# Kernel optimization log

Hardware: AMD Instinct MI355X
Metric: run time of the kernel (lower is better)

The kernel has to match this reference:

```python
import jax, jax.numpy as jnp
import numpy as np

S = 8192  # sequence length
D = 256   # feature dim


def setup_inputs() -> dict:
    key = jax.random.key(0)
    kq, kk, kv = jax.random.split(key, 3)
    Q = jax.random.normal(kq, (S, D), dtype=jnp.float32)
    K = jax.random.normal(kk, (S, D), dtype=jnp.float32)
    V = jax.random.normal(kv, (S, D), dtype=jnp.float32)
    return {"Q": Q, "K": K, "V": V}


def reference(Q, K, V):
    # Faithful to the torch module: dk = K.size(-2) (the SEQUENCE length, not head dim)
    dk = K.shape[-2]
    scores = (Q @ K.T) / jnp.sqrt(jnp.float32(dk))  # [S, S]
    # F.softmax with implicit dim on a 2D tensor -> softmax over last dim (keys)
    attn = jax.nn.softmax(scores, axis=-1)
    return attn @ V  # [S, D]
```

## Files before the change

### kernel.cpp

```cpp
#include <hip/hip_runtime.h>


typedef __attribute__((ext_vector_type(4))) float    f32x4;
typedef __attribute__((ext_vector_type(4))) int      i32x4;
typedef __attribute__((ext_vector_type(2))) long     lx2;
typedef __attribute__((ext_vector_type(2))) _Float16 h2;
typedef __attribute__((ext_vector_type(2))) __fp16   h2raw;
typedef __attribute__((ext_vector_type(8))) _Float16 h8;
typedef long  __attribute__((may_alias)) long_a;
typedef lx2   __attribute__((may_alias)) lx2_a;
typedef h8    __attribute__((may_alias)) h8_a;

#define SEQ 8192
#define DIM 256
#define NSPLIT 8
#define KPS (SEQ / NSPLIT)
#define BN 32
#define ITERS (KPS / BN)
#define BM 128

#define KSC (1.4426950408889634f / 90.50966799187808f)

#define KTILE 8192
#define VTILE 16384
#define BUFSZ (KTILE + VTILE)

__global__ void __launch_bounds__(256)
prep(const float* __restrict__ Q, const float* __restrict__ K,
     const float* __restrict__ V, unsigned char* __restrict__ Q8,
     unsigned char* __restrict__ K8, _Float16* __restrict__ Vt) {
    __shared__ _Float16 tile[32][264];
    int b = blockIdx.x, t = threadIdx.x;

    {
        int row = b * 32 + (t >> 3);
        int c0 = (t & 7) * 8;
        const f32x4* q4 = (const f32x4*)Q + (size_t)row * 64 + c0;
        const f32x4* k4 = (const f32x4*)K + (size_t)row * 64 + c0;
        int qo[8], ko[8];
        #pragma unroll
        for (int i = 0; i < 8; ++i) {
            f32x4 q = q4[i], k = k4[i];
            int dq = 0, dk = 0;
            dq = __builtin_amdgcn_cvt_pk_fp8_f32(q.x, q.y, dq, false);
            dq = __builtin_amdgcn_cvt_pk_fp8_f32(q.z, q.w, dq, true);
            dk = __builtin_amdgcn_cvt_pk_fp8_f32(k.x, k.y, dk, false);
            dk = __builtin_amdgcn_cvt_pk_fp8_f32(k.z, k.w, dk, true);
            qo[i] = dq; ko[i] = dk;
        }
        i32x4* qd = (i32x4*)(Q8 + (size_t)row * 256 + (t & 7) * 32);
        qd[0] = *(i32x4*)&qo[0]; qd[1] = *(i32x4*)&qo[4];

        int s16h = (((t & 7) >> 1) << 1) + (t >> 7);
        long* kdst = (long*)(K8 + (size_t)b * KTILE + (size_t)s16h * 1024
                             + (size_t)((t >> 3) & 15) * 16 + (size_t)(t & 1) * 8);
        #pragma unroll
        for (int q = 0; q < 4; ++q) kdst[q * 32] = *(const long*)&ko[2 * q];
    }

    #pragma unroll
    for (int i = 0; i < 8; ++i) {
        int c = t + i * 256;
        int row = c >> 6, col = c & 63;
        f32x4 v = ((const f32x4*)V)[(size_t)(b * 32 + row) * 64 + col];
        tile[row][col * 4 + 0] = (_Float16)v.x;
        tile[row][col * 4 + 1] = (_Float16)v.y;
        tile[row][col * 4 + 2] = (_Float16)v.z;
        tile[row][col * 4 + 3] = (_Float16)v.w;
    }
    __syncthreads();
    _Float16* dst = Vt + (size_t)b * 8192 + (size_t)t * 8;
    #pragma unroll
    for (int a = 0; a < 4; ++a) {
        h8 w;
        #pragma unroll
        for (int j = 0; j < 4; ++j) {
            w[j]     = tile[4 * a + j][t];
            w[4 + j] = tile[16 + 4 * a + j][t];
        }
        *(h8_a*)(dst + (size_t)a * 2048) = w;
    }
}

__device__ __forceinline__ void gl16(const void* g, void* l) {
    __builtin_amdgcn_global_load_lds(
        (const __attribute__((address_space(1))) void*)g,
        (__attribute__((address_space(3))) void*)l, 16, 0, 0);
}

__device__ __forceinline__ h2 pkrtz(float a, float b) {
    h2raw r = __builtin_amdgcn_cvt_pkrtz(a, b);
    return __builtin_bit_cast(h2, r);
}

__device__ __forceinline__ void qk32(const unsigned char* kb, int koff,
                                     const long (&qf)[2][8], f32x4 (&sc)[2][2]) {
    #pragma unroll
    for (int h = 0; h < 2; ++h)
        #pragma unroll
        for (int t = 0; t < 2; ++t) sc[h][t] = (f32x4){0.f, 0.f, 0.f, 0.f};
    #pragma unroll
    for (int s16 = 0; s16 < 4; ++s16) {
        #pragma unroll
        for (int h = 0; h < 2; ++h) {
            lx2 kp = *(const lx2_a*)(kb + (s16 * 2 + h) * 1024 + koff);
            #pragma unroll
            for (int t = 0; t < 2; ++t) {
                sc[h][t] = __builtin_amdgcn_mfma_f32_16x16x32_fp8_fp8(kp[0], qf[t][2 * s16],     sc[h][t], 0, 0, 0);
                sc[h][t] = __builtin_amdgcn_mfma_f32_16x16x32_fp8_fp8(kp[1], qf[t][2 * s16 + 1], sc[h][t], 0, 0, 0);
            }
        }
    }
}

#define STAGE(KG, VG, BUF)                                                   \
    do {                                                                     \
        gl16((KG) + tid * 16,           (BUF) + wb);                         \
        gl16((KG) + 4096 + tid * 16,    (BUF) + 4096 + wb);                  \
        gl16((VG) + tid * 16,           (BUF) + KTILE + wb);                 \
        gl16((VG) + 4096 + tid * 16,    (BUF) + KTILE + 4096 + wb);         \
        gl16((VG) + 8192 + tid * 16,    (BUF) + KTILE + 8192 + wb);         \
        gl16((VG) + 12288 + tid * 16,   (BUF) + KTILE + 12288 + wb);        \
    } while (0)

__global__ void __launch_bounds__(256, 2)
attn(const unsigned char* __restrict__ Q8, const unsigned char* __restrict__ K8,
     const _Float16* __restrict__ Vt, _Float16* __restrict__ Op,
     float* __restrict__ lp) {
    __shared__ __align__(16) unsigned char lds[3 * BUFSZ];

    int tid = threadIdx.x;
    int wid = tid >> 6, lane = tid & 63;
    int l15 = lane & 15, qq = lane >> 4;
    int wb = wid << 10;
    int qt_blk = blockIdx.x >> 3, sp = blockIdx.x & 7;
    int qrow0 = qt_blk * BM + wid * 32;

    long qf[2][8];
    #pragma unroll
    for (int t = 0; t < 2; ++t) {
        const unsigned char* p = Q8 + (size_t)(qrow0 + t * 16 + l15) * DIM + qq * 8;
        #pragma unroll
        for (int s = 0; s < 8; ++s) qf[t][s] = *(const long_a*)(p + s * 32);
    }

    _Float16 one = (l15 == 0) ? (_Float16)1.0f : (_Float16)0.0f;
    h8 of = {one, one, one, one, one, one, one, one};

    unsigned char* bufA = lds;
    unsigned char* bufB = lds + BUFSZ;
    unsigned char* bufC = lds + 2 * BUFSZ;

    const unsigned char* kg = K8 + (size_t)sp * ITERS * KTILE;
    const unsigned char* vg = (const unsigned char*)Vt + (size_t)sp * ITERS * VTILE;

    f32x4 acc[2][16] = {};
    f32x4 accl[2] = {};

    int koff = qq * 256 + l15 * 16;
    int voff = qq * 4096 + l15 * 16;

    STAGE(kg, vg, bufA); kg += KTILE; vg += VTILE;
    STAGE(kg, vg, bufB); kg += KTILE; vg += VTILE;
    __syncthreads();
    f32x4 sc_p[2][2];
    qk32(bufA, koff, qf, sc_p);

    for (int it = 0; it < ITERS; ++it) {
        if (it + 2 < ITERS) { STAGE(kg, vg, bufC); kg += KTILE; vg += VTILE; }

        __builtin_amdgcn_s_setprio(1);

        f32x4 sc_n[2][2] = {};
        if (it + 1 < ITERS) qk32(bufB, koff, qf, sc_n);

        h8 pfrag[2];
        #pragma unroll
        for (int t = 0; t < 2; ++t) {
            float e0 = __builtin_amdgcn_exp2f(fminf(sc_p[0][t][0] * KSC, 16.0f));
            float e1 = __builtin_amdgcn_exp2f(fminf(sc_p[0][t][1] * KSC, 16.0f));
            float e2 = __builtin_amdgcn_exp2f(fminf(sc_p[0][t][2] * KSC, 16.0f));
            float e3 = __builtin_amdgcn_exp2f(fminf(sc_p[0][t][3] * KSC, 16.0f));
            float e4 = __builtin_amdgcn_exp2f(fminf(sc_p[1][t][0] * KSC, 16.0f));
            float e5 = __builtin_amdgcn_exp2f(fminf(sc_p[1][t][1] * KSC, 16.0f));
            float e6 = __builtin_amdgcn_exp2f(fminf(sc_p[1][t][2] * KSC, 16.0f));
            float e7 = __builtin_amdgcn_exp2f(fminf(sc_p[1][t][3] * KSC, 16.0f));
            h2 p01 = pkrtz(e0, e1);
            h2 p23 = pkrtz(e2, e3);
            h2 p45 = pkrtz(e4, e5);
            h2 p67 = pkrtz(e6, e7);
            h8 pf;
            pf[0] = p01[0]; pf[1] = p01[1]; pf[2] = p23[0]; pf[3] = p23[1];
            pf[4] = p45[0]; pf[5] = p45[1]; pf[6] = p67[0]; pf[7] = p67[1];
            pfrag[t] = pf;
        }

        const unsigned char* vb = bufA + KTILE + voff;
        #pragma unroll
        for (int n = 0; n < 16; ++n) {
            h8 vf = *(const h8_a*)(vb + n * 256);
            acc[0][n] = __builtin_amdgcn_mfma_f32_16x16x32_f16(pfrag[0], vf, acc[0][n], 0, 0, 0);
            acc[1][n] = __builtin_amdgcn_mfma_f32_16x16x32_f16(pfrag[1], vf, acc[1][n], 0, 0, 0);
        }
        accl[0] = __builtin_amdgcn_mfma_f32_16x16x32_f16(pfrag[0], of, accl[0], 0, 0, 0);
        accl[1] = __builtin_amdgcn_mfma_f32_16x16x32_f16(pfrag[1], of, accl[1], 0, 0, 0);

        __builtin_amdgcn_s_setprio(0);
        __syncthreads();

        unsigned char* tb = bufA; bufA = bufB; bufB = bufC; bufC = tb;
        #pragma unroll
        for (int h = 0; h < 2; ++h)
            #pragma unroll
            for (int t = 0; t < 2; ++t) sc_p[h][t] = sc_n[h][t];
    }

    #pragma unroll
    for (int t = 0; t < 2; ++t) {
        #pragma unroll
        for (int n = 0; n < 16; ++n)
            #pragma unroll
            for (int r = 0; r < 4; ++r) {
                int row = qrow0 + t * 16 + qq * 4 + r;
                Op[((size_t)sp * SEQ + row) * DIM + n * 16 + l15] = (_Float16)acc[t][n][r];
            }
        if (l15 == 0) {
            #pragma unroll
            for (int r = 0; r < 4; ++r)
                lp[(size_t)sp * SEQ + qrow0 + t * 16 + qq * 4 + r] = accl[t][r];
        }
    }
}

__global__ void __launch_bounds__(256)
combine(const _Float16* __restrict__ Op, const float* __restrict__ lp,
        float* __restrict__ out) {
    int idx = blockIdx.x * 256 + threadIdx.x;
    int row = idx >> 5;
    f32x4 a0 = {}, a1 = {};
    float l = 0.0f;
    #pragma unroll
    for (int s = 0; s < NSPLIT; ++s) {
        h8 h = *(const h8_a*)(Op + (size_t)s * SEQ * DIM + (size_t)idx * 8);
        a0.x += (float)h[0]; a0.y += (float)h[1];
        a0.z += (float)h[2]; a0.w += (float)h[3];
        a1.x += (float)h[4]; a1.y += (float)h[5];
        a1.z += (float)h[6]; a1.w += (float)h[7];
        l += lp[s * SEQ + row];
    }
    float linv = 1.0f / (l + 1e-20f);
    ((f32x4*)out)[idx * 2]     = a0 * linv;
    ((f32x4*)out)[idx * 2 + 1] = a1 * linv;
}

extern "C" void kernel_launch(void* const* d_in, const int* in_sizes, int n_in,
                              void* d_out, int out_size, void* d_ws, size_t ws_size,
                              hipStream_t stream) {
    const float* Q = (const float*)d_in[0];
    const float* K = (const float*)d_in[1];
    const float* V = (const float*)d_in[2];
    float* out = (float*)d_out;

    char* ws = (char*)d_ws;
    unsigned char* Q8 = (unsigned char*)ws;
    unsigned char* K8 = (unsigned char*)(ws + (2u << 20));
    _Float16* Vt = (_Float16*)(ws + (4u << 20));
    _Float16* Op = (_Float16*)(ws + (8u << 20));
    float*    lp = (float*)(ws + (40u << 20));

    prep   <<<256, 256, 0, stream>>>(Q, K, V, Q8, K8, Vt);
    attn   <<<NSPLIT * (SEQ / BM), 256, 0, stream>>>(Q8, K8, Vt, Op, lp);
    combine<<<1024, 256, 0, stream>>>(Op, lp, out);
}
```

Measured before the change: 140.0 us.

## Fuse split-K combine into attention via atomic last-block reduction, use 8 waves

Removes the separate combine kernel. The last split block for each query tile, detected with an atomic counter that prep zeroes, performs the reduction and writes the output. The attention block goes from 4 to 8 waves with 16 query rows per wave, uses double buffering instead of triple, and drops the software-pipelined QK score prefetch. This saves a kernel launch and raises occupancy, at the cost of less overlap between QK and PV inside each wave and a serialized reduction tail in the last block.

```diff
diff --git a/kernel.cpp b/kernel.cpp
--- a/kernel.cpp
+++ b/kernel.cpp
@@ -28,9 +28,12 @@
 __global__ void __launch_bounds__(256)
 prep(const float* __restrict__ Q, const float* __restrict__ K,
      const float* __restrict__ V, unsigned char* __restrict__ Q8,
-     unsigned char* __restrict__ K8, _Float16* __restrict__ Vt) {
+     unsigned char* __restrict__ K8, _Float16* __restrict__ Vt,
+     int* __restrict__ cnt) {
     __shared__ _Float16 tile[32][264];
     int b = blockIdx.x, t = threadIdx.x;
+
+    if (b == 0 && t < 64) cnt[t] = 0;
 
     {
         int row = b * 32 + (t >> 3);
@@ -93,164 +96,136 @@
     return __builtin_bit_cast(h2, r);
 }
 
-__device__ __forceinline__ void qk32(const unsigned char* kb, int koff,
-                                     const long (&qf)[2][8], f32x4 (&sc)[2][2]) {
-    #pragma unroll
-    for (int h = 0; h < 2; ++h)
-        #pragma unroll
-        for (int t = 0; t < 2; ++t) sc[h][t] = (f32x4){0.f, 0.f, 0.f, 0.f};
-    #pragma unroll
-    for (int s16 = 0; s16 < 4; ++s16) {
-        #pragma unroll
-        for (int h = 0; h < 2; ++h) {
-            lx2 kp = *(const lx2_a*)(kb + (s16 * 2 + h) * 1024 + koff);
-            #pragma unroll
-            for (int t = 0; t < 2; ++t) {
-                sc[h][t] = __builtin_amdgcn_mfma_f32_16x16x32_fp8_fp8(kp[0], qf[t][2 * s16],     sc[h][t], 0, 0, 0);
-                sc[h][t] = __builtin_amdgcn_mfma_f32_16x16x32_fp8_fp8(kp[1], qf[t][2 * s16 + 1], sc[h][t], 0, 0, 0);
-            }
-        }
-    }
-}
-
 #define STAGE(KG, VG, BUF)                                                   \
     do {                                                                     \
-        gl16((KG) + tid * 16,           (BUF) + wb);                         \
-        gl16((KG) + 4096 + tid * 16,    (BUF) + 4096 + wb);                  \
-        gl16((VG) + tid * 16,           (BUF) + KTILE + wb);                 \
-        gl16((VG) + 4096 + tid * 16,    (BUF) + KTILE + 4096 + wb);         \
-        gl16((VG) + 8192 + tid * 16,    (BUF) + KTILE + 8192 + wb);         \
-        gl16((VG) + 12288 + tid * 16,   (BUF) + KTILE + 12288 + wb);        \
+        gl16((KG) + tid * 16,          (BUF) + wb);                          \
+        gl16((VG) + tid * 16,          (BUF) + KTILE + wb);                  \
+        gl16((VG) + 8192 + tid * 16,   (BUF) + KTILE + 8192 + wb);          \
     } while (0)
 
-__global__ void __launch_bounds__(256, 2)
+__global__ void __launch_bounds__(512, 4)
 attn(const unsigned char* __restrict__ Q8, const unsigned char* __restrict__ K8,
      const _Float16* __restrict__ Vt, _Float16* __restrict__ Op,
-     float* __restrict__ lp) {
-    __shared__ __align__(16) unsigned char lds[3 * BUFSZ];
+     float* __restrict__ lp, float* __restrict__ out, int* __restrict__ cnt) {
+    __shared__ __align__(16) unsigned char lds[2 * BUFSZ];
+    __shared__ int lastv;
 
     int tid = threadIdx.x;
     int wid = tid >> 6, lane = tid & 63;
     int l15 = lane & 15, qq = lane >> 4;
     int wb = wid << 10;
     int qt_blk = blockIdx.x >> 3, sp = blockIdx.x & 7;
-    int qrow0 = qt_blk * BM + wid * 32;
-
-    long qf[2][8];
-    #pragma unroll
-    for (int t = 0; t < 2; ++t) {
-        const unsigned char* p = Q8 + (size_t)(qrow0 + t * 16 + l15) * DIM + qq * 8;
-        #pragma unroll
-        for (int s = 0; s < 8; ++s) qf[t][s] = *(const long_a*)(p + s * 32);
+    int qrow0 = qt_blk * BM + wid * 16;
+
+    long qf[8];
+    {
+        const unsigned char* p = Q8 + (size_t)(qrow0 + l15) * DIM + qq * 8;
+        #pragma unroll
+        for (int s = 0; s < 8; ++s) qf[s] = *(const long_a*)(p + s * 32);
     }
 
     _Float16 one = (l15 == 0) ? (_Float16)1.0f : (_Float16)0.0f;
     h8 of = {one, one, one, one, one, one, one, one};
 
-    unsigned char* bufA = lds;
-    unsigned char* bufB = lds + BUFSZ;
-    unsigned char* bufC = lds + 2 * BUFSZ;
-
     const unsigned char* kg = K8 + (size_t)sp * ITERS * KTILE;
     const unsigned char* vg = (const unsigned char*)Vt + (size_t)sp * ITERS * VTILE;
 
-    f32x4 acc[2][16] = {};
-    f32x4 accl[2] = {};
+    f32x4 acc[16] = {};
+    f32x4 accl = {};
 
     int koff = qq * 256 + l15 * 16;
     int voff = qq * 4096 + l15 * 16;
 
-    STAGE(kg, vg, bufA); kg += KTILE; vg += VTILE;
-    STAGE(kg, vg, bufB); kg += KTILE; vg += VTILE;
-    __syncthreads();
-    f32x4 sc_p[2][2];
-    qk32(bufA, koff, qf, sc_p);
+    STAGE(kg, vg, lds); kg += KTILE; vg += VTILE;
+    __syncthreads();
 
     for (int it = 0; it < ITERS; ++it) {
-        if (it + 2 < ITERS) { STAGE(kg, vg, bufC); kg += KTILE; vg += VTILE; }
+        unsigned char* buf = lds + (it & 1) * BUFSZ;
+        if (it + 1 < ITERS) {
+            STAGE(kg, vg, lds + ((it + 1) & 1) * BUFSZ);
+            kg += KTILE; vg += VTILE;
+        }
 
         __builtin_amdgcn_s_setprio(1);
 
-        f32x4 sc_n[2][2] = {};
-        if (it + 1 < ITERS) qk32(bufB, koff, qf, sc_n);
-
-        h8 pfrag[2];
-        #pragma unroll
-        for (int t = 0; t < 2; ++t) {
-            float e0 = __builtin_amdgcn_exp2f(fminf(sc_p[0][t][0] * KSC, 16.0f));
-            float e1 = __builtin_amdgcn_exp2f(fminf(sc_p[0][t][1] * KSC, 16.0f));
-            float e2 = __builtin_amdgcn_exp2f(fminf(sc_p[0][t][2] * KSC, 16.0f));
-            float e3 = __builtin_amdgcn_exp2f(fminf(sc_p[0][t][3] * KSC, 16.0f));
-            float e4 = __builtin_amdgcn_exp2f(fminf(sc_p[1][t][0] * KSC, 16.0f));
-            float e5 = __builtin_amdgcn_exp2f(fminf(sc_p[1][t][1] * KSC, 16.0f));
-            float e6 = __builtin_amdgcn_exp2f(fminf(sc_p[1][t][2] * KSC, 16.0f));
-            float e7 = __builtin_amdgcn_exp2f(fminf(sc_p[1][t][3] * KSC, 16.0f));
-            h2 p01 = pkrtz(e0, e1);
-            h2 p23 = pkrtz(e2, e3);
-            h2 p45 = pkrtz(e4, e5);
-            h2 p67 = pkrtz(e6, e7);
-            h8 pf;
-            pf[0] = p01[0]; pf[1] = p01[1]; pf[2] = p23[0]; pf[3] = p23[1];
-            pf[4] = p45[0]; pf[5] = p45[1]; pf[6] = p67[0]; pf[7] = p67[1];
-            pfrag[t] = pf;
-        }
-
-        const unsigned char* vb = bufA + KTILE + voff;
+        f32x4 sc[2] = {};
+        #pragma unroll
+        for (int s16 = 0; s16 < 4; ++s16) {
+            #pragma unroll
+            for (int h = 0; h < 2; ++h) {
+                lx2 kp = *(const lx2_a*)(buf + (s16 * 2 + h) * 1024 + koff);
+                sc[h] = __builtin_amdgcn_mfma_f32_16x16x32_fp8_fp8(kp[0], qf[2 * s16],     sc[h], 0, 0, 0);
+                sc[h] = __builtin_amdgcn_mfma_f32_16x16x32_fp8_fp8(kp[1], qf[2 * s16 + 1], sc[h], 0, 0, 0);
+            }
+        }
+
+        float e0 = __builtin_amdgcn_exp2f(fminf(sc[0][0] * KSC, 16.0f));
+        float e1 = __builtin_amdgcn_exp2f(fminf(sc[0][1] * KSC, 16.0f));
+        float e2 = __builtin_amdgcn_exp2f(fminf(sc[0][2] * KSC, 16.0f));
+        float e3 = __builtin_amdgcn_exp2f(fminf(sc[0][3] * KSC, 16.0f));
+        float e4 = __builtin_amdgcn_exp2f(fminf(sc[1][0] * KSC, 16.0f));
+        float e5 = __builtin_amdgcn_exp2f(fminf(sc[1][1] * KSC, 16.0f));
+        float e6 = __builtin_amdgcn_exp2f(fminf(sc[1][2] * KSC, 16.0f));
+        float e7 = __builtin_amdgcn_exp2f(fminf(sc[1][3] * KSC, 16.0f));
+        h2 p01 = pkrtz(e0, e1);
+        h2 p23 = pkrtz(e2, e3);
+        h2 p45 = pkrtz(e4, e5);
+        h2 p67 = pkrtz(e6, e7);
+        h8 pfrag;
+        pfrag[0] = p01[0]; pfrag[1] = p01[1]; pfrag[2] = p23[0]; pfrag[3] = p23[1];
+        pfrag[4] = p45[0]; pfrag[5] = p45[1]; pfrag[6] = p67[0]; pfrag[7] = p67[1];
+
+        const unsigned char* vb = buf + KTILE + voff;
         #pragma unroll
         for (int n = 0; n < 16; ++n) {
             h8 vf = *(const h8_a*)(vb + n * 256);
-            acc[0][n] = __builtin_amdgcn_mfma_f32_16x16x32_f16(pfrag[0], vf, acc[0][n], 0, 0, 0);
-            acc[1][n] = __builtin_amdgcn_mfma_f32_16x16x32_f16(pfrag[1], vf, acc[1][n], 0, 0, 0);
-        }
-        accl[0] = __builtin_amdgcn_mfma_f32_16x16x32_f16(pfrag[0], of, accl[0], 0, 0, 0);
-        accl[1] = __builtin_amdgcn_mfma_f32_16x16x32_f16(pfrag[1], of, accl[1], 0, 0, 0);
+            acc[n] = __builtin_amdgcn_mfma_f32_16x16x32_f16(pfrag, vf, acc[n], 0, 0, 0);
+        }
+        accl = __builtin_amdgcn_mfma_f32_16x16x32_f16(pfrag, of, accl, 0, 0, 0);
 
         __builtin_amdgcn_s_setprio(0);
         __syncthreads();
-
-        unsigned char* tb = bufA; bufA = bufB; bufB = bufC; bufC = tb;
-        #pragma unroll
-        for (int h = 0; h < 2; ++h)
+    }
+
+    #pragma unroll
+    for (int n = 0; n < 16; ++n)
+        #pragma unroll
+        for (int r = 0; r < 4; ++r) {
+            int row = qrow0 + qq * 4 + r;
+            Op[((size_t)sp * SEQ + row) * DIM + n * 16 + l15] = (_Float16)acc[n][r];
+        }
+    if (l15 == 0) {
+        #pragma unroll
+        for (int r = 0; r < 4; ++r)
+            lp[(size_t)sp * SEQ + qrow0 + qq * 4 + r] = accl[r];
+    }
+
+    __threadfence();
+    __syncthreads();
+    if (tid == 0) lastv = atomicAdd(cnt + qt_blk, 1);
+    __syncthreads();
+    if (lastv == NSPLIT - 1) {
+        __threadfence();
+        #pragma unroll 1
+        for (int c = 0; c < 8; ++c) {
+            int idx = (qt_blk << 12) + (c << 9) + tid;
+            int row = idx >> 5;
+            f32x4 a0 = {}, a1 = {};
+            float l = 0.0f;
             #pragma unroll
-            for (int t = 0; t < 2; ++t) sc_p[h][t] = sc_n[h][t];
-    }
-
-    #pragma unroll
-    for (int t = 0; t < 2; ++t) {
-        #pragma unroll
-        for (int n = 0; n < 16; ++n)
-            #pragma unroll
-            for (int r = 0; r < 4; ++r) {
-                int row = qrow0 + t * 16 + qq * 4 + r;
-                Op[((size_t)sp * SEQ + row) * DIM + n * 16 + l15] = (_Float16)acc[t][n][r];
+            for (int s = 0; s < NSPLIT; ++s) {
+                h8 h = *(const h8_a*)(Op + (size_t)s * SEQ * DIM + (size_t)idx * 8);
+                a0.x += (float)h[0]; a0.y += (float)h[1];
+                a0.z += (float)h[2]; a0.w += (float)h[3];
+                a1.x += (float)h[4]; a1.y += (float)h[5];
+                a1.z += (float)h[6]; a1.w += (float)h[7];
+                l += lp[s * SEQ + row];
             }
-        if (l15 == 0) {
-            #pragma unroll
-            for (int r = 0; r < 4; ++r)
-                lp[(size_t)sp * SEQ + qrow0 + t * 16 + qq * 4 + r] = accl[t][r];
-        }
-    }
-}
-
-__global__ void __launch_bounds__(256)
-combine(const _Float16* __restrict__ Op, const float* __restrict__ lp,
-        float* __restrict__ out) {
-    int idx = blockIdx.x * 256 + threadIdx.x;
-    int row = idx >> 5;
-    f32x4 a0 = {}, a1 = {};
-    float l = 0.0f;
-    #pragma unroll
-    for (int s = 0; s < NSPLIT; ++s) {
-        h8 h = *(const h8_a*)(Op + (size_t)s * SEQ * DIM + (size_t)idx * 8);
-        a0.x += (float)h[0]; a0.y += (float)h[1];
-        a0.z += (float)h[2]; a0.w += (float)h[3];
-        a1.x += (float)h[4]; a1.y += (float)h[5];
-        a1.z += (float)h[6]; a1.w += (float)h[7];
-        l += lp[s * SEQ + row];
-    }
-    float linv = 1.0f / (l + 1e-20f);
-    ((f32x4*)out)[idx * 2]     = a0 * linv;
-    ((f32x4*)out)[idx * 2 + 1] = a1 * linv;
+            float linv = 1.0f / (l + 1e-20f);
+            ((f32x4*)out)[(size_t)idx * 2]     = a0 * linv;
+            ((f32x4*)out)[(size_t)idx * 2 + 1] = a1 * linv;
+        }
+    }
 }
 
 extern "C" void kernel_launch(void* const* d_in, const int* in_sizes, int n_in,
@@ -267,8 +242,8 @@
     _Float16* Vt = (_Float16*)(ws + (4u << 20));
     _Float16* Op = (_Float16*)(ws + (8u << 20));
     float*    lp = (float*)(ws + (40u << 20));
-
-    prep   <<<256, 256, 0, stream>>>(Q, K, V, Q8, K8, Vt);
-    attn   <<<NSPLIT * (SEQ / BM), 256, 0, stream>>>(Q8, K8, Vt, Op, lp);
-    combine<<<1024, 256, 0, stream>>>(Op, lp, out);
-}
+    int*     cnt = (int*)(ws + (40u << 20) + (256u << 10));
+
+    prep<<<256, 256, 0, stream>>>(Q, K, V, Q8, K8, Vt, cnt);
+    attn<<<NSPLIT * (SEQ / BM), 512, 0, stream>>>(Q8, K8, Vt, Op, lp, out, cnt);
+}
```

Measured after the change: 340.2 us. +142.9%, slower.

## Fuse split-K combine into attention kernel via last-block atomic counter

Applied to the files above, without the earlier changes.

Removes the separate combine launch. Each attention block increments a per-query-tile atomic counter after writing its partial output, and the last of the NSPLIT blocks reduces all partials for that tile and writes the final normalized output. Counters are zeroed in the prep kernel. This saves a kernel launch and lets combine work overlap with other tiles' attention, but the last block per tile now does serial reduction work with only 256 threads, which could create a tail.

```diff
diff --git a/kernel.cpp b/kernel.cpp
--- a/kernel.cpp
+++ b/kernel.cpp
@@ -28,9 +28,12 @@
 __global__ void __launch_bounds__(256)
 prep(const float* __restrict__ Q, const float* __restrict__ K,
      const float* __restrict__ V, unsigned char* __restrict__ Q8,
-     unsigned char* __restrict__ K8, _Float16* __restrict__ Vt) {
+     unsigned char* __restrict__ K8, _Float16* __restrict__ Vt,
+     int* __restrict__ cnt) {
     __shared__ _Float16 tile[32][264];
     int b = blockIdx.x, t = threadIdx.x;
+
+    if (b == 0 && t < 64) cnt[t] = 0;
 
     {
         int row = b * 32 + (t >> 3);
@@ -126,8 +129,9 @@
 __global__ void __launch_bounds__(256, 2)
 attn(const unsigned char* __restrict__ Q8, const unsigned char* __restrict__ K8,
      const _Float16* __restrict__ Vt, _Float16* __restrict__ Op,
-     float* __restrict__ lp) {
+     float* __restrict__ lp, float* __restrict__ out, int* __restrict__ cnt) {
     __shared__ __align__(16) unsigned char lds[3 * BUFSZ];
+    __shared__ int lastv;
 
     int tid = threadIdx.x;
     int wid = tid >> 6, lane = tid & 63;
@@ -230,27 +234,33 @@
                 lp[(size_t)sp * SEQ + qrow0 + t * 16 + qq * 4 + r] = accl[t][r];
         }
     }
-}
-
-__global__ void __launch_bounds__(256)
-combine(const _Float16* __restrict__ Op, const float* __restrict__ lp,
-        float* __restrict__ out) {
-    int idx = blockIdx.x * 256 + threadIdx.x;
-    int row = idx >> 5;
-    f32x4 a0 = {}, a1 = {};
-    float l = 0.0f;
-    #pragma unroll
-    for (int s = 0; s < NSPLIT; ++s) {
-        h8 h = *(const h8_a*)(Op + (size_t)s * SEQ * DIM + (size_t)idx * 8);
-        a0.x += (float)h[0]; a0.y += (float)h[1];
-        a0.z += (float)h[2]; a0.w += (float)h[3];
-        a1.x += (float)h[4]; a1.y += (float)h[5];
-        a1.z += (float)h[6]; a1.w += (float)h[7];
-        l += lp[s * SEQ + row];
-    }
-    float linv = 1.0f / (l + 1e-20f);
-    ((f32x4*)out)[idx * 2]     = a0 * linv;
-    ((f32x4*)out)[idx * 2 + 1] = a1 * linv;
+
+    __threadfence();
+    __syncthreads();
+    if (tid == 0) lastv = atomicAdd(cnt + qt_blk, 1);
+    __syncthreads();
+    if (lastv == NSPLIT - 1) {
+        __threadfence();
+        #pragma unroll 1
+        for (int c = 0; c < 16; ++c) {
+            int idx = (qt_blk << 12) + (c << 8) + tid;
+            int row = idx >> 5;
+            f32x4 a0 = {}, a1 = {};
+            float l = 0.0f;
+            #pragma unroll
+            for (int s = 0; s < NSPLIT; ++s) {
+                h8 h = *(const h8_a*)(Op + (size_t)s * SEQ * DIM + (size_t)idx * 8);
+                a0.x += (float)h[0]; a0.y += (float)h[1];
+                a0.z += (float)h[2]; a0.w += (float)h[3];
+                a1.x += (float)h[4]; a1.y += (float)h[5];
+                a1.z += (float)h[6]; a1.w += (float)h[7];
+                l += lp[s * SEQ + row];
+            }
+            float linv = 1.0f / (l + 1e-20f);
+            ((f32x4*)out)[(size_t)idx * 2]     = a0 * linv;
+            ((f32x4*)out)[(size_t)idx * 2 + 1] = a1 * linv;
+        }
+    }
 }
 
 extern "C" void kernel_launch(void* const* d_in, const int* in_sizes, int n_in,
@@ -267,8 +277,8 @@
     _Float16* Vt = (_Float16*)(ws + (4u << 20));
     _Float16* Op = (_Float16*)(ws + (8u << 20));
     float*    lp = (float*)(ws + (40u << 20));
-
-    prep   <<<256, 256, 0, stream>>>(Q, K, V, Q8, K8, Vt);
-    attn   <<<NSPLIT * (SEQ / BM), 256, 0, stream>>>(Q8, K8, Vt, Op, lp);
-    combine<<<1024, 256, 0, stream>>>(Op, lp, out);
-}
+    int*     cnt = (int*)(ws + (40u << 20) + (256u << 10));
+
+    prep<<<256, 256, 0, stream>>>(Q, K, V, Q8, K8, Vt, cnt);
+    attn<<<NSPLIT * (SEQ / BM), 256, 0, stream>>>(Q8, K8, Vt, Op, lp, out, cnt);
+}
```

Result: slower. 246.2 us (+75.9%).

## Load K tiles directly into registers instead of staging through LDS

Applied to the files above, without the earlier changes.

K fragments are now read from global memory straight into registers (prefetched one iteration ahead), and only V tiles are staged into LDS through the triple buffer. This cuts the LDS footprint and the LDS read traffic for the QK MFMAs, and drops the sc_p/sc_n copy by reordering softmax before the next QK. In exchange it adds register pressure from the K prefetch registers and exposes global load latency directly to the waves.

```diff
diff --git a/kernel.cpp b/kernel.cpp
--- a/kernel.cpp
+++ b/kernel.cpp
@@ -23,7 +23,6 @@
 
 #define KTILE 8192
 #define VTILE 16384
-#define BUFSZ (KTILE + VTILE)
 
 __global__ void __launch_bounds__(256)
 prep(const float* __restrict__ Q, const float* __restrict__ K,
@@ -93,8 +92,15 @@
     return __builtin_bit_cast(h2, r);
 }
 
-__device__ __forceinline__ void qk32(const unsigned char* kb, int koff,
-                                     const long (&qf)[2][8], f32x4 (&sc)[2][2]) {
+__device__ __forceinline__ void loadk(const unsigned char* kg, int koff,
+                                      lx2 (&kreg)[8]) {
+    #pragma unroll
+    for (int c = 0; c < 8; ++c)
+        kreg[c] = *(const lx2_a*)(kg + c * 1024 + koff);
+}
+
+__device__ __forceinline__ void qk32r(const lx2 (&kreg)[8], const long (&qf)[2][8],
+                                      f32x4 (&sc)[2][2]) {
     #pragma unroll
     for (int h = 0; h < 2; ++h)
         #pragma unroll
@@ -103,7 +109,7 @@
     for (int s16 = 0; s16 < 4; ++s16) {
         #pragma unroll
         for (int h = 0; h < 2; ++h) {
-            lx2 kp = *(const lx2_a*)(kb + (s16 * 2 + h) * 1024 + koff);
+            lx2 kp = kreg[s16 * 2 + h];
             #pragma unroll
             for (int t = 0; t < 2; ++t) {
                 sc[h][t] = __builtin_amdgcn_mfma_f32_16x16x32_fp8_fp8(kp[0], qf[t][2 * s16],     sc[h][t], 0, 0, 0);
@@ -113,21 +119,53 @@
     }
 }
 
-#define STAGE(KG, VG, BUF)                                                   \
+__device__ __forceinline__ void sm32(const f32x4 (&sc)[2][2], h8 (&pfrag)[2]) {
+    #pragma unroll
+    for (int t = 0; t < 2; ++t) {
+        float e0 = __builtin_amdgcn_exp2f(fminf(sc[0][t][0] * KSC, 16.0f));
+        float e1 = __builtin_amdgcn_exp2f(fminf(sc[0][t][1] * KSC, 16.0f));
+        float e2 = __builtin_amdgcn_exp2f(fminf(sc[0][t][2] * KSC, 16.0f));
+        float e3 = __builtin_amdgcn_exp2f(fminf(sc[0][t][3] * KSC, 16.0f));
+        float e4 = __builtin_amdgcn_exp2f(fminf(sc[1][t][0] * KSC, 16.0f));
+        float e5 = __builtin_amdgcn_exp2f(fminf(sc[1][t][1] * KSC, 16.0f));
+        float e6 = __builtin_amdgcn_exp2f(fminf(sc[1][t][2] * KSC, 16.0f));
+        float e7 = __builtin_amdgcn_exp2f(fminf(sc[1][t][3] * KSC, 16.0f));
+        h2 p01 = pkrtz(e0, e1);
+        h2 p23 = pkrtz(e2, e3);
+        h2 p45 = pkrtz(e4, e5);
+        h2 p67 = pkrtz(e6, e7);
+        h8 pf;
+        pf[0] = p01[0]; pf[1] = p01[1]; pf[2] = p23[0]; pf[3] = p23[1];
+        pf[4] = p45[0]; pf[5] = p45[1]; pf[6] = p67[0]; pf[7] = p67[1];
+        pfrag[t] = pf;
+    }
+}
+
+__device__ __forceinline__ void pv32(const unsigned char* vb, const h8 (&pfrag)[2],
+                                     const h8& of, f32x4 (&acc)[2][16], f32x4 (&accl)[2]) {
+    #pragma unroll
+    for (int n = 0; n < 16; ++n) {
+        h8 vf = *(const h8_a*)(vb + n * 256);
+        acc[0][n] = __builtin_amdgcn_mfma_f32_16x16x32_f16(pfrag[0], vf, acc[0][n], 0, 0, 0);
+        acc[1][n] = __builtin_amdgcn_mfma_f32_16x16x32_f16(pfrag[1], vf, acc[1][n], 0, 0, 0);
+    }
+    accl[0] = __builtin_amdgcn_mfma_f32_16x16x32_f16(pfrag[0], of, accl[0], 0, 0, 0);
+    accl[1] = __builtin_amdgcn_mfma_f32_16x16x32_f16(pfrag[1], of, accl[1], 0, 0, 0);
+}
+
+#define STAGEV(VG, BUF)                                                      \
     do {                                                                     \
-        gl16((KG) + tid * 16,           (BUF) + wb);                         \
-        gl16((KG) + 4096 + tid * 16,    (BUF) + 4096 + wb);                  \
-        gl16((VG) + tid * 16,           (BUF) + KTILE + wb);                 \
-        gl16((VG) + 4096 + tid * 16,    (BUF) + KTILE + 4096 + wb);         \
-        gl16((VG) + 8192 + tid * 16,    (BUF) + KTILE + 8192 + wb);         \
-        gl16((VG) + 12288 + tid * 16,   (BUF) + KTILE + 12288 + wb);        \
+        gl16((VG) + tid * 16,          (BUF) + wb);                          \
+        gl16((VG) + 4096 + tid * 16,   (BUF) + 4096 + wb);                   \
+        gl16((VG) + 8192 + tid * 16,   (BUF) + 8192 + wb);                   \
+        gl16((VG) + 12288 + tid * 16,  (BUF) + 12288 + wb);                  \
     } while (0)
 
 __global__ void __launch_bounds__(256, 2)
 attn(const unsigned char* __restrict__ Q8, const unsigned char* __restrict__ K8,
      const _Float16* __restrict__ Vt, _Float16* __restrict__ Op,
      float* __restrict__ lp) {
-    __shared__ __align__(16) unsigned char lds[3 * BUFSZ];
+    __shared__ __align__(16) unsigned char lds[3 * VTILE];
 
     int tid = threadIdx.x;
     int wid = tid >> 6, lane = tid & 63;
@@ -148,8 +186,8 @@
     h8 of = {one, one, one, one, one, one, one, one};
 
     unsigned char* bufA = lds;
-    unsigned char* bufB = lds + BUFSZ;
-    unsigned char* bufC = lds + 2 * BUFSZ;
+    unsigned char* bufB = lds + VTILE;
+    unsigned char* bufC = lds + 2 * VTILE;
 
     const unsigned char* kg = K8 + (size_t)sp * ITERS * KTILE;
     const unsigned char* vg = (const unsigned char*)Vt + (size_t)sp * ITERS * VTILE;
@@ -160,59 +198,34 @@
     int koff = qq * 256 + l15 * 16;
     int voff = qq * 4096 + l15 * 16;
 
-    STAGE(kg, vg, bufA); kg += KTILE; vg += VTILE;
-    STAGE(kg, vg, bufB); kg += KTILE; vg += VTILE;
+    lx2 kreg[8];
+
+    STAGEV(vg, bufA); vg += VTILE;
+    STAGEV(vg, bufB); vg += VTILE;
+    loadk(kg, koff, kreg); kg += KTILE;
     __syncthreads();
-    f32x4 sc_p[2][2];
-    qk32(bufA, koff, qf, sc_p);
+    f32x4 sc[2][2];
+    qk32r(kreg, qf, sc);
+    loadk(kg, koff, kreg); kg += KTILE;
 
     for (int it = 0; it < ITERS; ++it) {
-        if (it + 2 < ITERS) { STAGE(kg, vg, bufC); kg += KTILE; vg += VTILE; }
+        if (it + 2 < ITERS) { STAGEV(vg, bufC); vg += VTILE; }
 
         __builtin_amdgcn_s_setprio(1);
 
-        f32x4 sc_n[2][2] = {};
-        if (it + 1 < ITERS) qk32(bufB, koff, qf, sc_n);
-
         h8 pfrag[2];
-        #pragma unroll
-        for (int t = 0; t < 2; ++t) {
-            float e0 = __builtin_amdgcn_exp2f(fminf(sc_p[0][t][0] * KSC, 16.0f));
-            float e1 = __builtin_amdgcn_exp2f(fminf(sc_p[0][t][1] * KSC, 16.0f));
-            float e2 = __builtin_amdgcn_exp2f(fminf(sc_p[0][t][2] * KSC, 16.0f));
-            float e3 = __builtin_amdgcn_exp2f(fminf(sc_p[0][t][3] * KSC, 16.0f));
-            float e4 = __builtin_amdgcn_exp2f(fminf(sc_p[1][t][0] * KSC, 16.0f));
-            float e5 = __builtin_amdgcn_exp2f(fminf(sc_p[1][t][1] * KSC, 16.0f));
-            float e6 = __builtin_amdgcn_exp2f(fminf(sc_p[1][t][2] * KSC, 16.0f));
-            float e7 = __builtin_amdgcn_exp2f(fminf(sc_p[1][t][3] * KSC, 16.0f));
-            h2 p01 = pkrtz(e0, e1);
-            h2 p23 = pkrtz(e2, e3);
-            h2 p45 = pkrtz(e4, e5);
-            h2 p67 = pkrtz(e6, e7);
-            h8 pf;
-            pf[0] = p01[0]; pf[1] = p01[1]; pf[2] = p23[0]; pf[3] = p23[1];
-            pf[4] = p45[0]; pf[5] = p45[1]; pf[6] = p67[0]; pf[7] = p67[1];
-            pfrag[t] = pf;
-        }
-
-        const unsigned char* vb = bufA + KTILE + voff;
-        #pragma unroll
-        for (int n = 0; n < 16; ++n) {
-            h8 vf = *(const h8_a*)(vb + n * 256);
-            acc[0][n] = __builtin_amdgcn_mfma_f32_16x16x32_f16(pfrag[0], vf, acc[0][n], 0, 0, 0);
-            acc[1][n] = __builtin_amdgcn_mfma_f32_16x16x32_f16(pfrag[1], vf, acc[1][n], 0, 0, 0);
-        }
-        accl[0] = __builtin_amdgcn_mfma_f32_16x16x32_f16(pfrag[0], of, accl[0], 0, 0, 0);
-        accl[1] = __builtin_amdgcn_mfma_f32_16x16x32_f16(pfrag[1], of, accl[1], 0, 0, 0);
+        sm32(sc, pfrag);
+
+        if (it + 1 < ITERS) qk32r(kreg, qf, sc);
+
+        if (it + 2 < ITERS) { loadk(kg, koff, kreg); kg += KTILE; }
+
+        pv32(bufA + voff, pfrag, of, acc, accl);
 
         __builtin_amdgcn_s_setprio(0);
         __syncthreads();
 
         unsigned char* tb = bufA; bufA = bufB; bufB = bufC; bufC = tb;
-        #pragma unroll
-        for (int h = 0; h < 2; ++h)
-            #pragma unroll
-            for (int t = 0; t < 2; ++t) sc_p[h][t] = sc_n[h][t];
     }
 
     #pragma unroll
```

New measurement: 140.4 us. About the same (+0.3%).
